# Kernel optimization log

Measured on AMD Instinct MI355X. Metric: run time of the kernel, lower is better.

The kernel has to match this reference:

```python
import jax, jax.numpy as jnp
import numpy as np

T = 32768          # number of t_eval points, dt = 30 s
BATCH = 32         # batched initial conditions
N_ROOMS = 16
N_STATE = N_ROOMS + 2
HID = 16
T0 = 259200.0      # start time (seconds); kept small so fp32 resolves 30 s steps
DT_GRID = 30.0
MU, STD = 23.359, 1.41      # state normalization for policy input
Q_VALUE = -16914.0          # cooling power per unit action
DAY = 86400.0
WEEK = 604800.0
A_SCALE, A_DIAG, B_SCALE = 1e-4, 1e-3, 1e-6


def setup_inputs() -> dict:
    key = jax.random.key(0)
    ks = jax.random.split(key, 8)
    t_eval = (T0 + DT_GRID * jnp.arange(T)).astype(jnp.float32)
    iv = 26.0 + jax.random.normal(ks[0], (BATCH, N_STATE), jnp.float32)
    W_A = jax.random.normal(ks[1], (N_STATE, N_STATE), jnp.float32)
    W_B = jax.random.normal(ks[2], (N_STATE, 1 + N_ROOMS), jnp.float32)
    W1 = jax.random.normal(ks[3], (HID, N_STATE + 2), jnp.float32)
    b1 = jax.random.normal(ks[4], (HID,), jnp.float32)
    w2 = jax.random.normal(ks[5], (HID,), jnp.float32)
    b2 = jax.random.normal(ks[6], (1,), jnp.float32)
    # outside-temperature table on a 30 s grid covering t_eval plus the +600 s tail
    Tout_table = 10.0 + 10.0 * jax.random.uniform(ks[7], (T + 21,), jnp.float32)
    return dict(t_eval=t_eval, iv=iv, W_A=W_A, W_B=W_B, W1=W1, b1=b1,
                w2=w2, b2=b2, Tout_table=Tout_table)


def reference(t_eval, iv, W_A, W_B, W1, b1, w2, b2, Tout_table):
    n = iv.shape[-1]
    A = A_SCALE * W_A - A_DIAG * jnp.eye(n, dtype=W_A.dtype)   # stable dynamics
    Bm = B_SCALE * W_B                                         # [n, 1+n_rooms]
    b_tout = Bm[:, 0]                                          # Tout column of B
    b_rooms = Q_VALUE * jnp.sum(Bm[:, 1:], axis=1)             # B @ (Q*ones) per unit action
    t0 = t_eval[0]
    nT = Tout_table.shape[0]

    def tout(t):  # linear interp of outside temperature at absolute time t
        pos = (t - t0) / DT_GRID
        i = jnp.clip(jnp.floor(pos).astype(jnp.int32), 0, nT - 2)
        fr = pos - i.astype(pos.dtype)
        return (1.0 - fr) * Tout_table[i] + fr * Tout_table[i + 1]

    def policy(t, x):  # deterministic cooling action in (0,1), per batch element
        tod = jnp.mod(t, DAY) / DAY
        tow = jnp.mod(t + 3.0 * DAY, WEEK) / WEEK   # epoch day 0 is a Thursday
        feats = jnp.broadcast_to(jnp.stack([tow, tod]).astype(x.dtype), (x.shape[0], 2))
        s = jnp.concatenate([(x - MU) / STD, feats], axis=1)   # [B, n+2]
        h = jnp.tanh(s @ W1.T + b1)
        return jax.nn.sigmoid(h @ w2 + b2[0])                  # [B]

    def f(t, x, act):  # dx/dt = A x + B u,  u = [Tout, Q*ones(n_rooms)]
        Bu = tout(t) * b_tout[None, :] + act[:, None] * b_rooms[None, :]
        return x @ A.T + Bu

    def step(x, ts):  # one fixed-step RK4 step; action held over the step (>=30 s gate)
        t, tn = ts
        dt = tn - t
        act = policy(t, x)
        k1 = f(t, x, act)
        k2 = f(t + 0.5 * dt, x + 0.5 * dt * k1, act)
        k3 = f(t + 0.5 * dt, x + 0.5 * dt * k2, act)
        k4 = f(tn, x + dt * k3, act)
        xn = x + (dt / 6.0) * (k1 + 2.0 * k2 + 2.0 * k3 + k4)
        return xn, xn

    _, xs = jax.lax.scan(step, iv, (t_eval[:-1], t_eval[1:]))
    return jnp.concatenate([iv[None], xs], axis=0)   # [T, batch, n_state]
```

## Files before the change

### kernel.cpp

```cpp
#include <hip/hip_runtime.h>

#define NSTATE 18
#define NBATCH 32
#define TSTEPS 32768
#define BURN   176

#define RSEGS   128
#define RSEGLEN 256
#define FSEGS   64
#define FSEGLEN 512

typedef float v2f __attribute__((ext_vector_type(2)));

#define EXP2F(x) __builtin_amdgcn_exp2f(x)

#define PKFMA_LO(ACC, Gp, Xp) \
  asm("v_pk_fma_f32 %0, %1, %2, %0 op_sel:[0,0,0] op_sel_hi:[1,0,1]" \
      : "+v"(ACC) : "v"(Gp), "v"(Xp))
#define PKFMA_HI(ACC, Gp, Xp) \
  asm("v_pk_fma_f32 %0, %1, %2, %0 op_sel:[0,1,0] op_sel_hi:[1,1,1]" \
      : "+v"(ACC) : "v"(Gp), "v"(Xp))

template <int CTRL>
__device__ __forceinline__ float dpp_xadd(float x) {
  int y = __builtin_amdgcn_update_dpp(0, __float_as_int(x), CTRL, 0xF, 0xF, true);
  return x + __int_as_float(y);
}

#define STEPP(XI, XO, TIN, TNX, P, DOSTORE)                                       \
  do {                                                                            \
    TNX = *(const v2f*)(ldsT + 2 * (P) + 2);          \
    v2f accA; accA.x = 0.0f; accA.y = 0.0f;                                       \
    v2f accB; accB.x = 0.0f; accB.y = 0.0f;                                       \
    PKFMA_LO(accA, G[0],  XI[0]);  PKFMA_HI(accB, G[1],  XI[0]);                  \
    PKFMA_LO(accA, G[2],  XI[1]);  PKFMA_HI(accB, G[3],  XI[1]);                  \
    PKFMA_LO(accA, G[4],  XI[2]);  PKFMA_HI(accB, G[5],  XI[2]);                  \
    PKFMA_LO(accA, G[6],  XI[3]);  PKFMA_HI(accB, G[7],  XI[3]);                  \
    PKFMA_LO(accA, G[8],  XI[4]);  PKFMA_HI(accB, G[9],  XI[4]);                  \
    PKFMA_LO(accA, G[10], XI[5]);  PKFMA_HI(accB, G[11], XI[5]);                  \
    PKFMA_LO(accA, G[12], XI[6]);  PKFMA_HI(accB, G[13], XI[6]);                  \
    PKFMA_LO(accA, G[14], XI[7]);  PKFMA_HI(accB, G[15], XI[7]);                  \
    PKFMA_LO(accA, G[16], XI[8]);  PKFMA_HI(accB, G[17], XI[8]);                  \
    float tb = fmaf((float)(P), dtw, CBase);                                      \
    float clo = fmaf(TIN.x, C0.x, fmaf(TIN.y, C1.x, tb));                         \
    clo = fmaf(TNX.x, C2lo, clo);                                                 \
    clo = fmaf(a0p, F0.x, clo);             \
    clo = fmaf(a1p, F1.x, clo);                                                   \
    float chi = fmaf(TIN.x, C0.y, TIN.y * C1.y);                                  \
    chi = fmaf(a0p, F0.y, chi);                                                   \
    chi = fmaf(a1p, F1.y, chi);                                                   \
    v2f acc = accA + accB;                                                        \
    float vlo = acc.x + clo, vhi = acc.y + chi;                                   \
    xbuf[wIdx] = vlo;              \
    XO[0] = *(const v2f*)(xbuf + 0);  XO[1] = *(const v2f*)(xbuf + 2);            \
    XO[2] = *(const v2f*)(xbuf + 4);  XO[3] = *(const v2f*)(xbuf + 6);            \
    XO[4] = *(const v2f*)(xbuf + 8);  XO[5] = *(const v2f*)(xbuf + 10);           \
    XO[6] = *(const v2f*)(xbuf + 12); XO[7] = *(const v2f*)(xbuf + 14);           \
    XO[8] = *(const v2f*)(xbuf + 16);                                             \
    float e2 = EXP2F(vlo);                                                        \
    float rc = __builtin_amdgcn_rcpf(1.0f + e2);                                  \
    float pA = fmaf(nw2A, rc, w2A);                                               \
    pA = dpp_xadd<0xB1>(pA); pA = dpp_xadd<0x4E>(pA);                             \
    pA = dpp_xadd<0x141>(pA); pA = dpp_xadd<0x140>(pA);                           \
    float ez = EXP2F(fmaf(pA, -1.44269504f, nb2));                                \
    float an = __builtin_amdgcn_rcpf(1.0f + ez);                                  \
    float aj0 = __int_as_float(__builtin_amdgcn_readlane(__float_as_int(an), 32));\
    float qB = fmaf(aj0, uB, vlo);                                                \
    float e2b = EXP2F(qB);                                                        \
    float rcb = __builtin_amdgcn_rcpf(1.0f + e2b);                                \
    float pB = fmaf(nw2B, rcb, w2B);                                              \
    pB = dpp_xadd<0xB1>(pB); pB = dpp_xadd<0x4E>(pB);                             \
    pB = dpp_xadd<0x141>(pB); pB = dpp_xadd<0x140>(pB);                           \
    float ezb = EXP2F(fmaf(pB, -1.44269504f, nb2));                               \
    float anb = __builtin_amdgcn_rcpf(1.0f + ezb);                                \
    float aj1 = __int_as_float(__builtin_amdgcn_readlane(__float_as_int(anb), 48));\
    if (DOSTORE) {                                                                \
      if (L < NSTATE) {                                                           \
        ob[L] = fmaf(aj0, cact, vhi);                               \
        ob[L + 576] = fmaf(aj1, cact, fmaf(aj0, pcact, vlo));       \
      }                                                                            \
      ob += 1152;                                                                 \
    }                                                                             \
    a0p = aj0; a1p = aj1;                                                         \
  } while (0)

#define TWRAP(P)                                                                  \
  do {                                                                            \
    if ((P) + 1 == pD) CBase -= dayCorr;                                          \
    if ((P) + 1 == pW) CBase -= weekCorr;                                         \
  } while (0)

#define SETUP_BODY(DBp, WA, WB, W1, b1, w2, NT)                                    \
  double* A   = DBp;                                     \
  double* A2  = DBp + 324;                           \
  double* A3  = DBp + 648;                                                         \
  double* A4  = DBp + 972;                                                         \
  double* bt  = DBp + 1296;                                                        \
  double* br  = DBp + 1314;                                                        \
  double* cv  = DBp + 1332;                                                        \
  double* d0v = DBp + 1350;                                                        \
  double* d1v = DBp + 1368;                                                        \
  double* pc1 = DBp + 1386;                                                        \
  double* pc2 = DBp + 1404;                                                        \
  double* pc3 = DBp + 1422;                                                        \
  const double dt = 30.0;                                                          \
  for (int t = L; t < 324; t += NT) {                                              \
    int i = t / 18, j = t % 18;                                                    \
    A[t] = 1e-4 * (double)WA[t] - (i == j ? 1e-3 : 0.0);                           \
  }                                                                                \
  if (L < NSTATE) {                                                                \
    bt[L] = 1e-6 * (double)WB[L * 17 + 0];                                         \
    double ssum = 0.0;                                                             \
    for (int c = 1; c < 17; ++c) ssum += (double)WB[L * 17 + c];                   \
    br[L] = -16914.0 * 1e-6 * ssum;                                                \
  }                                                                                \
  __syncthreads();                                                                 \
  for (int t = L; t < 324; t += NT) {                                              \
    int i = t / 18, j = t % 18;                                                    \
    double s2 = 0.0;                                                               \
    for (int l = 0; l < 18; ++l) s2 += A[i * 18 + l] * A[l * 18 + j];              \
    A2[t] = s2;                                                                    \
  }                                                                                \
  __syncthreads();                                                                 \
  for (int t = L; t < 324; t += NT) {                                              \
    int i = t / 18, j = t % 18;                                                    \
    double s3 = 0.0, s4 = 0.0;                                                     \
    for (int l = 0; l < 18; ++l) {                                                 \
      s3 += A2[i * 18 + l] * A[l * 18 + j];                                        \
      s4 += A2[i * 18 + l] * A2[l * 18 + j];                                       \
    }                                                                              \
    A3[t] = s3;                                                                    \
    A4[t] = s4;                                                                    \
  }                                                                                \
  __syncthreads();                                                                 \
  if (L < NSTATE) {                                                                \
    double sc = 0.0, dd0 = 0.0, dd1 = 0.0;                                         \
    for (int j = 0; j < 18; ++j) {                                                 \
      double m = (dt / 6.0) * ((L == j ? 6.0 : 0.0) + 3.0 * dt * A[L * 18 + j] +   \
                               dt * dt * A2[L * 18 + j] +                          \
                               0.25 * dt * dt * dt * A3[L * 18 + j]);              \
      sc += m * br[j];                                                             \
      double m1 = (dt / 6.0) * ((L == j ? 1.0 : 0.0) + dt * A[L * 18 + j] +        \
                                0.5 * dt * dt * A2[L * 18 + j] +                   \
                                0.25 * dt * dt * dt * A3[L * 18 + j]);             \
      double m23 = (dt / 6.0) * ((L == j ? 4.0 : 0.0) + 2.0 * dt * A[L * 18 + j] + \
                                 0.5 * dt * dt * A2[L * 18 + j]);                  \
      double m4 = (L == j ? dt / 6.0 : 0.0);                                       \
      dd0 += (m1 + 0.5 * m23) * bt[j];                                             \
      dd1 += (0.5 * m23 + m4) * bt[j];                                             \
    }                                                                              \
    cv[L] = sc;                                                                    \
    d0v[L] = dd0;                                                                  \
    d1v[L] = dd1;                                                                  \
  }                                                                                \
  __syncthreads();                                                                 \
  for (int t = L; t < 324; t += NT) {                                              \
    int i = t / 18, j = t % 18;                                                    \
    A[t] = (i == j ? 1.0 : 0.0) + dt * A[t] + (dt * dt / 2.0) * A2[t] +            \
           (dt * dt * dt / 6.0) * A3[t] + (dt * dt * dt * dt / 24.0) * A4[t];      \
  }                                                                                \
  __syncthreads();                                                                 \
  for (int t = L; t < 324; t += NT) {                                              \
    int i = t / 18, j = t % 18;                                                    \
    double s2 = 0.0;                                                               \
    for (int l = 0; l < 18; ++l) s2 += A[i * 18 + l] * A[l * 18 + j];              \
    A2[t] = s2;                                                                    \
  }                                                                                \
  __syncthreads();                                                                 \
  if (L < NSTATE) { double s1 = 0.0; for (int j = 0; j < 18; ++j) s1 += A[L * 18 + j] * cv[j];  pc1[L] = s1; } \
  __syncthreads();                                                                 \
  if (L < NSTATE) { double s1 = 0.0; for (int j = 0; j < 18; ++j) s1 += A[L * 18 + j] * pc1[j]; pc2[L] = s1; } \
  __syncthreads();                                                                 \
  if (L < NSTATE) { double s1 = 0.0; for (int j = 0; j < 18; ++j) s1 += A[L * 18 + j] * pc2[j]; pc3[L] = s1; } \
  __syncthreads();                                                                 \
  v2f G[18];                                                                       \
  v2f F0; F0.x = 0.f; F0.y = 0.f;                                                  \
  v2f F1; F1.x = 0.f; F1.y = 0.f;                                                  \
  v2f C0; C0.x = 0.f; C0.y = 0.f;                                                  \
  v2f C1; C1.x = 0.f; C1.y = 0.f;                                                  \
  float C2lo = 0.f, CWlo = 0.f, CTlo = 0.f, CBlo = 0.f;                            \
  float cact = 0.f, pcact = 0.f, uB = 0.f;                                         \
  float w2A = 0.f, nw2A = 0.f, w2B = 0.f, nw2B = 0.f;                              \
  if (L < NSTATE) {                                                                \
    for (int j = 0; j < 18; ++j) { G[j].x = (float)A2[L * 18 + j]; G[j].y = (float)A[L * 18 + j]; } \
    double pd0 = 0.0, pd1 = 0.0;                                                   \
    for (int j = 0; j < 18; ++j) { pd0 += A[L * 18 + j] * d0v[j]; pd1 += A[L * 18 + j] * d1v[j]; } \
    C0.x = (float)pd0;            C0.y = (float)d0v[L];                            \
    C1.x = (float)(pd1 + d0v[L]); C1.y = (float)d1v[L];                            \
    C2lo = (float)d1v[L];                                                          \
    F0.x = (float)pc3[L]; F0.y = (float)pc2[L];                                    \
    F1.x = (float)pc2[L]; F1.y = (float)pc1[L];                                    \
    cact = (float)cv[L];                                                           \
    pcact = (float)pc1[L];                                                         \
  } else if (L >= 32 && L < 48) {                                                  \
    int m = L - 32;                                                                \
    double f0 = 0.0, f1 = 0.0, ssum = 0.0;                                         \
    for (int j = 0; j < 18; ++j) {                                                 \
      double g = (double)W1[m * 20 + j] * ((double)PS / 1.41);                     \
      G[j].x = (float)g; G[j].y = 0.f;                                             \
      f0 += g * pc1[j];                                                            \
      f1 += g * cv[j];                                                             \
      ssum += (double)W1[m * 20 + j];                                              \
    }                                                                              \
    F0.x = (float)f0; F1.x = (float)f1;                                            \
    CBlo = (float)(((double)b1[m] - ssum * (23.359 / 1.41)) * (double)PS);         \
    CWlo = W1[m * 20 + 18] * PS * (1.0f / 604800.0f);                              \
    CTlo = W1[m * 20 + 19] * PS * (1.0f / 86400.0f);                               \
    w2A = w2[m]; nw2A = -2.0f * w2A;                                               \
  } else if (L >= 48 && L < 64) {                                                  \
    int m = L - 48;                                                                \
    double f0 = 0.0, f1 = 0.0, ub = 0.0, ssum = 0.0, wd0 = 0.0, wd1 = 0.0;         \
    for (int j = 0; j < 18; ++j) {                                                 \
      double g = (double)W1[m * 20 + j] * ((double)PS / 1.41);                     \
      double wp = 0.0;                                                             \
      for (int k = 0; k < 18; ++k)                                                 \
        wp += (double)W1[m * 20 + k] * ((double)PS / 1.41) * A[k * 18 + j];        \
      G[j].x = (float)wp; G[j].y = 0.f;                                            \
      f0 += g * pc2[j];                                                            \
      f1 += g * pc1[j];                                                            \
      ub += g * cv[j];                                                             \
      wd0 += g * d0v[j];                                                           \
      wd1 += g * d1v[j];                                                           \
      ssum += (double)W1[m * 20 + j];                                              \
    }                                                                              \
    F0.x = (float)f0; F1.x = (float)f1; uB = (float)ub;                            \
    C0.x = (float)wd0; C1.x = (float)wd1;                                          \
    CWlo = W1[m * 20 + 18] * PS * (1.0f / 604800.0f);                              \
    CTlo = W1[m * 20 + 19] * PS * (1.0f / 86400.0f);                               \
    CBlo = (float)(((double)b1[m] - ssum * (23.359 / 1.41)) * (double)PS) +        \
           30.0f * CWlo + 30.0f * CTlo;                                            \
    w2B = w2[m]; nw2B = -2.0f * w2B;                                               \
  } else {                                                                         \
    for (int j = 0; j < 18; ++j) { G[j].x = 0.f; G[j].y = 0.f; }                   \
  }

#define TIME_BASE_SETUP(kbv)                                                       \
  const unsigned ft0u = (30u * (unsigned)(kbv)) % 86400u;                          \
  const unsigned fw0u = (518400u + 30u * (unsigned)(kbv)) % 604800u;               \
  const int pD = (int)((86400u - ft0u + 59u) / 60u);                               \
  const int pW = (int)((604800u - fw0u + 59u) / 60u);                              \
  float CBase = fmaf((float)ft0u, CTlo, fmaf((float)fw0u, CWlo, CBlo));            \
  const float dtw = fmaf(60.0f, CTlo, 60.0f * CWlo);                               \
  const float dayCorr = 86400.0f * CTlo;                                           \
  const float weekCorr = 604800.0f * CWlo;

__global__ __launch_bounds__(256) void rc_setup(
    const float* __restrict__ WA, const float* __restrict__ WB,
    const float* __restrict__ W1, const float* __restrict__ b1,
    const float* __restrict__ w2, float* __restrict__ wsf) {
  __shared__ double DB[1440];
  const int L = threadIdx.x;
  const float PS = 2.88539008f;
  SETUP_BODY(DB, WA, WB, W1, b1, w2, 256);

  if (L < 64) {
#pragma unroll
    for (int j = 0; j < 18; ++j) *(v2f*)(wsf + j * 128 + 2 * L) = G[j];
    *(v2f*)(wsf + 2304 + 0 * 128 + 2 * L) = F0;
    *(v2f*)(wsf + 2304 + 1 * 128 + 2 * L) = F1;
    *(v2f*)(wsf + 2304 + 2 * 128 + 2 * L) = C0;
    *(v2f*)(wsf + 2304 + 3 * 128 + 2 * L) = C1;
    float* scp = wsf + 2816;
    scp[0 * 64 + L] = C2lo;  scp[1 * 64 + L] = CWlo;  scp[2 * 64 + L] = CTlo;
    scp[3 * 64 + L] = CBlo;  scp[4 * 64 + L] = cact;  scp[5 * 64 + L] = pcact;
    scp[6 * 64 + L] = uB;    scp[7 * 64 + L] = w2A;   scp[8 * 64 + L] = nw2A;
    scp[9 * 64 + L] = w2B;   scp[10 * 64 + L] = nw2B;
  }
}

__global__ __launch_bounds__(64, 4) void rc_run(
    const float* __restrict__ ws, const float* __restrict__ b2,
    const float* __restrict__ iv, const float* __restrict__ tout,
    float* __restrict__ out) {
  __shared__ float ldsT[BURN + RSEGLEN + 2];
  __shared__ __align__(16) float xbuf[96];

  const int L = threadIdx.x;
  const int idx = blockIdx.x;
  const int b = idx & (NBATCH - 1);
  const int s = idx >> 5;

  const int ks = (s == RSEGS - 1) ? (TSTEPS - 1 - RSEGLEN) : s * RSEGLEN;
  const int kb = max(0, ks - BURN);
  const int mBurn = ks - kb;
  const int mEnd = (ks + RSEGLEN) - kb;

  v2f G[18];
#pragma unroll
  for (int j = 0; j < 18; ++j) G[j] = *(const v2f*)(ws + j * 128 + 2 * L);
  v2f F0 = *(const v2f*)(ws + 2304 + 0 * 128 + 2 * L);
  v2f F1 = *(const v2f*)(ws + 2304 + 1 * 128 + 2 * L);
  v2f C0 = *(const v2f*)(ws + 2304 + 2 * 128 + 2 * L);
  v2f C1 = *(const v2f*)(ws + 2304 + 3 * 128 + 2 * L);
  const float* scp = ws + 2816;
  const float C2lo = scp[0 * 64 + L], CWlo = scp[1 * 64 + L];
  const float CTlo = scp[2 * 64 + L], CBlo = scp[3 * 64 + L];
  const float cact = scp[4 * 64 + L], pcact = scp[5 * 64 + L];
  const float uB   = scp[6 * 64 + L];
  const float w2A  = scp[7 * 64 + L], nw2A = scp[8 * 64 + L];
  const float w2B  = scp[9 * 64 + L], nw2B = scp[10 * 64 + L];
  const float nb2 = -1.44269504f * b2[0];

  TIME_BASE_SETUP(kb);

  const int cnt = mEnd + 2;
  for (int i = L; i < cnt; i += 64) ldsT[i] = tout[kb + i];
  __syncthreads();

  float q = (L < NSTATE) ? iv[b * NSTATE + L] : 0.0f;
  if (s == 0 && L < NSTATE) out[b * NSTATE + L] = q;

  float a0p = 0.0f, a1p = 0.0f;

  float* ob = out + (size_t)(ks + 1) * (NBATCH * NSTATE) + b * NSTATE;

  const int wIdx = (L < NSTATE) ? L : (32 + L);
  xbuf[wIdx] = q;
  v2f X[9], Y[9];
  X[0] = *(const v2f*)(xbuf + 0);  X[1] = *(const v2f*)(xbuf + 2);
  X[2] = *(const v2f*)(xbuf + 4);  X[3] = *(const v2f*)(xbuf + 6);
  X[4] = *(const v2f*)(xbuf + 8);  X[5] = *(const v2f*)(xbuf + 10);
  X[6] = *(const v2f*)(xbuf + 12); X[7] = *(const v2f*)(xbuf + 14);
  X[8] = *(const v2f*)(xbuf + 16);

  v2f tU, tV;
  tU.x = ldsT[0]; tU.y = ldsT[1];

  const int nburn = mBurn >> 1;
  const int ntot = mEnd >> 1;
  int p = 0;
  for (; p < nburn; p += 2) {
    STEPP(X, Y, tU, tV, p, false);     TWRAP(p);
    STEPP(Y, X, tV, tU, p + 1, false); TWRAP(p + 1);
  }
  for (; p < ntot; p += 2) {
    STEPP(X, Y, tU, tV, p, true);      TWRAP(p);
    STEPP(Y, X, tV, tU, p + 1, true);  TWRAP(p + 1);
  }
}

__global__ __launch_bounds__(64, 2) void rc_fused(
    const float* __restrict__ WA, const float* __restrict__ WB,
    const float* __restrict__ W1, const float* __restrict__ b1,
    const float* __restrict__ w2, const float* __restrict__ b2,
    const float* __restrict__ iv, const float* __restrict__ tout,
    float* __restrict__ out) {
  __shared__ double DB[1440];
  __shared__ __align__(16) float xbuf[96];

  const int L = threadIdx.x;
  const int idx = blockIdx.x;
  const int b = idx & (NBATCH - 1);
  const int s = idx >> 5;
  const float PS = 2.88539008f;

  const int ks = (s == FSEGS - 1) ? (TSTEPS - 1 - FSEGLEN) : s * FSEGLEN;
  const int kb = max(0, ks - BURN);
  const int mBurn = ks - kb;
  const int mEnd = (ks + FSEGLEN) - kb;

  SETUP_BODY(DB, WA, WB, W1, b1, w2, 64);
  const float b2v = b2[0];
  const float nb2 = -1.44269504f * b2v;
  TIME_BASE_SETUP(kb);
  __syncthreads();

  float* ldsT = (float*)DB;
  const int cnt = mEnd + 2;
  for (int i = L; i < cnt; i += 64) ldsT[i] = tout[kb + i];
  __syncthreads();

  float q = (L < NSTATE) ? iv[b * NSTATE + L] : 0.0f;
  if (s == 0 && L < NSTATE) out[b * NSTATE + L] = q;

  float a0p = 0.0f, a1p = 0.0f;

  float* ob = out + (size_t)(ks + 1) * (NBATCH * NSTATE) + b * NSTATE;

  const int wIdx = (L < NSTATE) ? L : (32 + L);
  xbuf[wIdx] = q;
  v2f X[9], Y[9];
  X[0] = *(const v2f*)(xbuf + 0);  X[1] = *(const v2f*)(xbuf + 2);
  X[2] = *(const v2f*)(xbuf + 4);  X[3] = *(const v2f*)(xbuf + 6);
  X[4] = *(const v2f*)(xbuf + 8);  X[5] = *(const v2f*)(xbuf + 10);
  X[6] = *(const v2f*)(xbuf + 12); X[7] = *(const v2f*)(xbuf + 14);
  X[8] = *(const v2f*)(xbuf + 16);

  v2f tU, tV;
  tU.x = ldsT[0]; tU.y = ldsT[1];

  const int nburn = mBurn >> 1;
  const int ntot = mEnd >> 1;
  int p = 0;
  for (; p < nburn; p += 2) {
    STEPP(X, Y, tU, tV, p, false);     TWRAP(p);
    STEPP(Y, X, tV, tU, p + 1, false); TWRAP(p + 1);
  }
  for (; p < ntot; p += 2) {
    STEPP(X, Y, tU, tV, p, true);      TWRAP(p);
    STEPP(Y, X, tV, tU, p + 1, true);  TWRAP(p + 1);
  }
}

extern "C" void kernel_launch(void* const* d_in, const int* in_sizes, int n_in,
                              void* d_out, int out_size, void* d_ws, size_t ws_size,
                              hipStream_t stream) {
  const float* iv = (const float*)d_in[1];
  const float* WA = (const float*)d_in[2];
  const float* WB = (const float*)d_in[3];
  const float* W1 = (const float*)d_in[4];
  const float* b1 = (const float*)d_in[5];
  const float* w2 = (const float*)d_in[6];
  const float* b2 = (const float*)d_in[7];
  const float* tout = (const float*)d_in[8];
  float* out = (float*)d_out;

  if (d_ws != nullptr && ws_size >= 14336) {
    float* wsf = (float*)d_ws;
    rc_setup<<<1, 256, 0, stream>>>(WA, WB, W1, b1, w2, wsf);
    rc_run<<<NBATCH * RSEGS, 64, 0, stream>>>(wsf, b2, iv, tout, out);
  } else {
    rc_fused<<<NBATCH * FSEGS, 64, 0, stream>>>(WA, WB, W1, b1, w2, b2, iv, tout, out);
  }
}
```

Before: 228.6 us.

## Interleave two batch elements per wavefront in rc_run for ILP

```diff
diff --git a/kernel.cpp b/kernel.cpp
--- a/kernel.cpp
+++ b/kernel.cpp
@@ -27,9 +27,93 @@
   return x + __int_as_float(y);
 }
 
+#define POLICY(VLO, AJ0, AJ1)                                                     \
+    float e2_ = EXP2F(VLO);                                                       \
+    float rc_ = __builtin_amdgcn_rcpf(1.0f + e2_);                                \
+    float pA_ = fmaf(nw2A, rc_, w2A);                                             \
+    pA_ = dpp_xadd<0xB1>(pA_); pA_ = dpp_xadd<0x4E>(pA_);                         \
+    pA_ = dpp_xadd<0x141>(pA_); pA_ = dpp_xadd<0x140>(pA_);                       \
+    float ez_ = EXP2F(fmaf(pA_, -1.44269504f, nb2));                              \
+    float an_ = __builtin_amdgcn_rcpf(1.0f + ez_);                                \
+    AJ0 = __int_as_float(__builtin_amdgcn_readlane(__float_as_int(an_), 32));     \
+    float qB_ = fmaf(AJ0, uB, VLO);                                               \
+    float e2b_ = EXP2F(qB_);                                                      \
+    float rcb_ = __builtin_amdgcn_rcpf(1.0f + e2b_);                              \
+    float pB_ = fmaf(nw2B, rcb_, w2B);                                            \
+    pB_ = dpp_xadd<0xB1>(pB_); pB_ = dpp_xadd<0x4E>(pB_);                         \
+    pB_ = dpp_xadd<0x141>(pB_); pB_ = dpp_xadd<0x140>(pB_);                       \
+    float ezb_ = EXP2F(fmaf(pB_, -1.44269504f, nb2));                             \
+    float anb_ = __builtin_amdgcn_rcpf(1.0f + ezb_);                              \
+    AJ1 = __int_as_float(__builtin_amdgcn_readlane(__float_as_int(anb_), 48))
+
+#define STEPP2(XI0, XO0, XI1, XO1, TIN, TNX, P, DOSTORE)                          \
+  do {                                                                            \
+    TNX = *(const v2f*)(ldsT + 2 * (P) + 2);          \
+    v2f aA0; aA0.x = 0.0f; aA0.y = 0.0f;                                          \
+    v2f aB0; aB0.x = 0.0f; aB0.y = 0.0f;                                          \
+    v2f aA1; aA1.x = 0.0f; aA1.y = 0.0f;                                          \
+    v2f aB1; aB1.x = 0.0f; aB1.y = 0.0f;                                          \
+    PKFMA_LO(aA0, G[0],  XI0[0]);  PKFMA_HI(aB0, G[1],  XI0[0]);                  \
+    PKFMA_LO(aA1, G[0],  XI1[0]);  PKFMA_HI(aB1, G[1],  XI1[0]);                  \
+    PKFMA_LO(aA0, G[2],  XI0[1]);  PKFMA_HI(aB0, G[3],  XI0[1]);                  \
+    PKFMA_LO(aA1, G[2],  XI1[1]);  PKFMA_HI(aB1, G[3],  XI1[1]);                  \
+    PKFMA_LO(aA0, G[4],  XI0[2]);  PKFMA_HI(aB0, G[5],  XI0[2]);                  \
+    PKFMA_LO(aA1, G[4],  XI1[2]);  PKFMA_HI(aB1, G[5],  XI1[2]);                  \
+    PKFMA_LO(aA0, G[6],  XI0[3]);  PKFMA_HI(aB0, G[7],  XI0[3]);                  \
+    PKFMA_LO(aA1, G[6],  XI1[3]);  PKFMA_HI(aB1, G[7],  XI1[3]);                  \
+    PKFMA_LO(aA0, G[8],  XI0[4]);  PKFMA_HI(aB0, G[9],  XI0[4]);                  \
+    PKFMA_LO(aA1, G[8],  XI1[4]);  PKFMA_HI(aB1, G[9],  XI1[4]);                  \
+    PKFMA_LO(aA0, G[10], XI0[5]);  PKFMA_HI(aB0, G[11], XI0[5]);                  \
+    PKFMA_LO(aA1, G[10], XI1[5]);  PKFMA_HI(aB1, G[11], XI1[5]);                  \
+    PKFMA_LO(aA0, G[12], XI0[6]);  PKFMA_HI(aB0, G[13], XI0[6]);                  \
+    PKFMA_LO(aA1, G[12], XI1[6]);  PKFMA_HI(aB1, G[13], XI1[6]);                  \
+    PKFMA_LO(aA0, G[14], XI0[7]);  PKFMA_HI(aB0, G[15], XI0[7]);                  \
+    PKFMA_LO(aA1, G[14], XI1[7]);  PKFMA_HI(aB1, G[15], XI1[7]);                  \
+    PKFMA_LO(aA0, G[16], XI0[8]);  PKFMA_HI(aB0, G[17], XI0[8]);                  \
+    PKFMA_LO(aA1, G[16], XI1[8]);  PKFMA_HI(aB1, G[17], XI1[8]);                  \
+    float tb = fmaf((float)(P), dtw, CBase);                                      \
+    float cshare = fmaf(TIN.x, C0.x, fmaf(TIN.y, C1.x, tb));                      \
+    cshare = fmaf(TNX.x, C2lo, cshare);                                           \
+    float clo0 = fmaf(a0p0, F0.x, cshare); clo0 = fmaf(a1p0, F1.x, clo0);         \
+    float clo1 = fmaf(a0p1, F0.x, cshare); clo1 = fmaf(a1p1, F1.x, clo1);         \
+    float chs = fmaf(TIN.x, C0.y, TIN.y * C1.y);                                  \
+    float chi0 = fmaf(a0p0, F0.y, chs); chi0 = fmaf(a1p0, F1.y, chi0);            \
+    float chi1 = fmaf(a0p1, F0.y, chs); chi1 = fmaf(a1p1, F1.y, chi1);            \
+    v2f ac0 = aA0 + aB0;                                                          \
+    v2f ac1 = aA1 + aB1;                                                          \
+    float vlo0 = ac0.x + clo0, vhi0 = ac0.y + chi0;                               \
+    float vlo1 = ac1.x + clo1, vhi1 = ac1.y + chi1;                               \
+    xb0[wIdx] = vlo0;           \
+    XO0[0] = *(const v2f*)(xb0 + 0);  XO0[1] = *(const v2f*)(xb0 + 2);            \
+    XO0[2] = *(const v2f*)(xb0 + 4);  XO0[3] = *(const v2f*)(xb0 + 6);            \
+    XO0[4] = *(const v2f*)(xb0 + 8);  XO0[5] = *(const v2f*)(xb0 + 10);           \
+    XO0[6] = *(const v2f*)(xb0 + 12); XO0[7] = *(const v2f*)(xb0 + 14);           \
+    XO0[8] = *(const v2f*)(xb0 + 16);                                             \
+    xb1[wIdx] = vlo1;                                                             \
+    XO1[0] = *(const v2f*)(xb1 + 0);  XO1[1] = *(const v2f*)(xb1 + 2);            \
+    XO1[2] = *(const v2f*)(xb1 + 4);  XO1[3] = *(const v2f*)(xb1 + 6);            \
+    XO1[4] = *(const v2f*)(xb1 + 8);  XO1[5] = *(const v2f*)(xb1 + 10);           \
+    XO1[6] = *(const v2f*)(xb1 + 12); XO1[7] = *(const v2f*)(xb1 + 14);           \
+    XO1[8] = *(const v2f*)(xb1 + 16);                                             \
+    float aj00, aj10, aj01, aj11;                                                 \
+    { POLICY(vlo0, aj00, aj10); }                                                 \
+    { POLICY(vlo1, aj01, aj11); }                                                 \
+    if (DOSTORE) {                                                                \
+      if (L < NSTATE) {                                                           \
+        ob0[L] = fmaf(aj00, cact, vhi0);                                          \
+        ob0[L + 576] = fmaf(aj10, cact, fmaf(aj00, pcact, vlo0));                 \
+        ob1[L] = fmaf(aj01, cact, vhi1);                                          \
+        ob1[L + 576] = fmaf(aj11, cact, fmaf(aj01, pcact, vlo1));                 \
+      }                                                                            \
+      ob0 += 1152; ob1 += 1152;                                                   \
+    }                                                                             \
+    a0p0 = aj00; a1p0 = aj10;                                                     \
+    a0p1 = aj01; a1p1 = aj11;                                                     \
+  } while (0)
+
 #define STEPP(XI, XO, TIN, TNX, P, DOSTORE)                                       \
   do {                                                                            \
-    TNX = *(const v2f*)(ldsT + 2 * (P) + 2);          \
+    TNX = *(const v2f*)(ldsT + 2 * (P) + 2);                                      \
     v2f accA; accA.x = 0.0f; accA.y = 0.0f;                                       \
     v2f accB; accB.x = 0.0f; accB.y = 0.0f;                                       \
     PKFMA_LO(accA, G[0],  XI[0]);  PKFMA_HI(accB, G[1],  XI[0]);                  \
@@ -44,40 +128,25 @@
     float tb = fmaf((float)(P), dtw, CBase);                                      \
     float clo = fmaf(TIN.x, C0.x, fmaf(TIN.y, C1.x, tb));                         \
     clo = fmaf(TNX.x, C2lo, clo);                                                 \
-    clo = fmaf(a0p, F0.x, clo);             \
+    clo = fmaf(a0p, F0.x, clo);                                                   \
     clo = fmaf(a1p, F1.x, clo);                                                   \
     float chi = fmaf(TIN.x, C0.y, TIN.y * C1.y);                                  \
     chi = fmaf(a0p, F0.y, chi);                                                   \
     chi = fmaf(a1p, F1.y, chi);                                                   \
     v2f acc = accA + accB;                                                        \
     float vlo = acc.x + clo, vhi = acc.y + chi;                                   \
-    xbuf[wIdx] = vlo;              \
+    xbuf[wIdx] = vlo;                                                             \
     XO[0] = *(const v2f*)(xbuf + 0);  XO[1] = *(const v2f*)(xbuf + 2);            \
     XO[2] = *(const v2f*)(xbuf + 4);  XO[3] = *(const v2f*)(xbuf + 6);            \
     XO[4] = *(const v2f*)(xbuf + 8);  XO[5] = *(const v2f*)(xbuf + 10);           \
     XO[6] = *(const v2f*)(xbuf + 12); XO[7] = *(const v2f*)(xbuf + 14);           \
     XO[8] = *(const v2f*)(xbuf + 16);                                             \
-    float e2 = EXP2F(vlo);                                                        \
-    float rc = __builtin_amdgcn_rcpf(1.0f + e2);                                  \
-    float pA = fmaf(nw2A, rc, w2A);                                               \
-    pA = dpp_xadd<0xB1>(pA); pA = dpp_xadd<0x4E>(pA);                             \
-    pA = dpp_xadd<0x141>(pA); pA = dpp_xadd<0x140>(pA);                           \
-    float ez = EXP2F(fmaf(pA, -1.44269504f, nb2));                                \
-    float an = __builtin_amdgcn_rcpf(1.0f + ez);                                  \
-    float aj0 = __int_as_float(__builtin_amdgcn_readlane(__float_as_int(an), 32));\
-    float qB = fmaf(aj0, uB, vlo);                                                \
-    float e2b = EXP2F(qB);                                                        \
-    float rcb = __builtin_amdgcn_rcpf(1.0f + e2b);                                \
-    float pB = fmaf(nw2B, rcb, w2B);                                              \
-    pB = dpp_xadd<0xB1>(pB); pB = dpp_xadd<0x4E>(pB);                             \
-    pB = dpp_xadd<0x141>(pB); pB = dpp_xadd<0x140>(pB);                           \
-    float ezb = EXP2F(fmaf(pB, -1.44269504f, nb2));                               \
-    float anb = __builtin_amdgcn_rcpf(1.0f + ezb);                                \
-    float aj1 = __int_as_float(__builtin_amdgcn_readlane(__float_as_int(anb), 48));\
+    float aj0, aj1;                                                               \
+    { POLICY(vlo, aj0, aj1); }                                                    \
     if (DOSTORE) {                                                                \
       if (L < NSTATE) {                                                           \
-        ob[L] = fmaf(aj0, cact, vhi);                               \
-        ob[L + 576] = fmaf(aj1, cact, fmaf(aj0, pcact, vlo));       \
+        ob[L] = fmaf(aj0, cact, vhi);                                             \
+        ob[L + 576] = fmaf(aj1, cact, fmaf(aj0, pcact, vlo));                     \
       }                                                                            \
       ob += 1152;                                                                 \
     }                                                                             \
@@ -91,8 +160,8 @@
   } while (0)
 
 #define SETUP_BODY(DBp, WA, WB, W1, b1, w2, NT)                                    \
-  double* A   = DBp;                                     \
-  double* A2  = DBp + 324;                           \
+  double* A   = DBp;                                                               \
+  double* A2  = DBp + 324;                                                         \
   double* A3  = DBp + 648;                                                         \
   double* A4  = DBp + 972;                                                         \
   double* bt  = DBp + 1296;                                                        \
@@ -268,17 +337,19 @@
   }
 }
 
-__global__ __launch_bounds__(64, 4) void rc_run(
+__global__ __launch_bounds__(64, 2) void rc_run(
     const float* __restrict__ ws, const float* __restrict__ b2,
     const float* __restrict__ iv, const float* __restrict__ tout,
     float* __restrict__ out) {
   __shared__ float ldsT[BURN + RSEGLEN + 2];
-  __shared__ __align__(16) float xbuf[96];
+  __shared__ __align__(16) float xb0[96];
+  __shared__ __align__(16) float xb1[96];
 
   const int L = threadIdx.x;
   const int idx = blockIdx.x;
-  const int b = idx & (NBATCH - 1);
-  const int s = idx >> 5;
+  const int b0 = idx & 15;
+  const int b1i = b0 + 16;
+  const int s = idx >> 4;
 
   const int ks = (s == RSEGS - 1) ? (TSTEPS - 1 - RSEGLEN) : s * RSEGLEN;
   const int kb = max(0, ks - BURN);
@@ -307,21 +378,27 @@
   for (int i = L; i < cnt; i += 64) ldsT[i] = tout[kb + i];
   __syncthreads();
 
-  float q = (L < NSTATE) ? iv[b * NSTATE + L] : 0.0f;
-  if (s == 0 && L < NSTATE) out[b * NSTATE + L] = q;
-
-  float a0p = 0.0f, a1p = 0.0f;
-
-  float* ob = out + (size_t)(ks + 1) * (NBATCH * NSTATE) + b * NSTATE;
+  float q0 = (L < NSTATE) ? iv[b0 * NSTATE + L] : 0.0f;
+  float q1 = (L < NSTATE) ? iv[b1i * NSTATE + L] : 0.0f;
+  if (s == 0 && L < NSTATE) {
+    out[b0 * NSTATE + L] = q0;
+    out[b1i * NSTATE + L] = q1;
+  }
+
+  float a0p0 = 0.0f, a1p0 = 0.0f, a0p1 = 0.0f, a1p1 = 0.0f;
+
+  float* ob0 = out + (size_t)(ks + 1) * (NBATCH * NSTATE) + b0 * NSTATE;
+  float* ob1 = out + (size_t)(ks + 1) * (NBATCH * NSTATE) + b1i * NSTATE;
 
   const int wIdx = (L < NSTATE) ? L : (32 + L);
-  xbuf[wIdx] = q;
-  v2f X[9], Y[9];
-  X[0] = *(const v2f*)(xbuf + 0);  X[1] = *(const v2f*)(xbuf + 2);
-  X[2] = *(const v2f*)(xbuf + 4);  X[3] = *(const v2f*)(xbuf + 6);
-  X[4] = *(const v2f*)(xbuf + 8);  X[5] = *(const v2f*)(xbuf + 10);
-  X[6] = *(const v2f*)(xbuf + 12); X[7] = *(const v2f*)(xbuf + 14);
-  X[8] = *(const v2f*)(xbuf + 16);
+  xb0[wIdx] = q0;
+  xb1[wIdx] = q1;
+  v2f X0[9], Y0[9], X1[9], Y1[9];
+#pragma unroll
+  for (int j = 0; j < 9; ++j) {
+    X0[j] = *(const v2f*)(xb0 + 2 * j);
+    X1[j] = *(const v2f*)(xb1 + 2 * j);
+  }
 
   v2f tU, tV;
   tU.x = ldsT[0]; tU.y = ldsT[1];
@@ -330,12 +407,12 @@
   const int ntot = mEnd >> 1;
   int p = 0;
   for (; p < nburn; p += 2) {
-    STEPP(X, Y, tU, tV, p, false);     TWRAP(p);
-    STEPP(Y, X, tV, tU, p + 1, false); TWRAP(p + 1);
+    STEPP2(X0, Y0, X1, Y1, tU, tV, p, false);     TWRAP(p);
+    STEPP2(Y0, X0, Y1, X1, tV, tU, p + 1, false); TWRAP(p + 1);
   }
   for (; p < ntot; p += 2) {
-    STEPP(X, Y, tU, tV, p, true);      TWRAP(p);
-    STEPP(Y, X, tV, tU, p + 1, true);  TWRAP(p + 1);
+    STEPP2(X0, Y0, X1, Y1, tU, tV, p, true);      TWRAP(p);
+    STEPP2(Y0, X0, Y1, X1, tV, tU, p + 1, true);  TWRAP(p + 1);
   }
 }
 
@@ -380,11 +457,8 @@
   const int wIdx = (L < NSTATE) ? L : (32 + L);
   xbuf[wIdx] = q;
   v2f X[9], Y[9];
-  X[0] = *(const v2f*)(xbuf + 0);  X[1] = *(const v2f*)(xbuf + 2);
-  X[2] = *(const v2f*)(xbuf + 4);  X[3] = *(const v2f*)(xbuf + 6);
-  X[4] = *(const v2f*)(xbuf + 8);  X[5] = *(const v2f*)(xbuf + 10);
-  X[6] = *(const v2f*)(xbuf + 12); X[7] = *(const v2f*)(xbuf + 14);
-  X[8] = *(const v2f*)(xbuf + 16);
+#pragma unroll
+  for (int j = 0; j < 9; ++j) X[j] = *(const v2f*)(xbuf + 2 * j);
 
   v2f tU, tV;
   tU.x = ldsT[0]; tU.y = ldsT[1];
@@ -418,7 +492,7 @@
   if (d_ws != nullptr && ws_size >= 14336) {
     float* wsf = (float*)d_ws;
     rc_setup<<<1, 256, 0, stream>>>(WA, WB, W1, b1, w2, wsf);
-    rc_run<<<NBATCH * RSEGS, 64, 0, stream>>>(wsf, b2, iv, tout, out);
+    rc_run<<<RSEGS * (NBATCH / 2), 64, 0, stream>>>(wsf, b2, iv, tout, out);
   } else {
     rc_fused<<<NBATCH * FSEGS, 64, 0, stream>>>(WA, WB, W1, b1, w2, b2, iv, tout, out);
   }
```

Result: no change. 230.2 us (+0.7%).
